# Optimization experiments

Measured on AMD Instinct MI355X. Metric: run time of the kernel, lower is better.

## Reference

```python
import jax, jax.numpy as jnp
import numpy as np

B, T, H, QS = 32, 4096, 512, 512

def setup_inputs() -> dict:
    key = jax.random.key(0)
    k1, k2, k3, k4, k5 = jax.random.split(key, 5)
    query = jax.random.normal(k1, (B, 1, QS), dtype=jnp.float32)
    precomputed_key = jax.random.normal(k2, (B, T, H), dtype=jnp.float32)
    value = jax.random.normal(k3, (B, T, H), dtype=jnp.float32)
    mask = jnp.ones((B, T), dtype=bool)  # unused in original forward
    Wq = jax.random.normal(k4, (H, QS), dtype=jnp.float32) * (1.0 / np.sqrt(QS))
    We = jax.random.normal(k5, (H,), dtype=jnp.float32) * (1.0 / np.sqrt(H))
    return {"query": query, "precomputed_key": precomputed_key, "value": value,
            "mask": mask, "Wq": Wq, "We": We}

def reference(query, precomputed_key, value, mask, Wq, We):
    # query_layer: Linear(query_size -> hidden, no bias): x @ Wq.T
    q = jnp.einsum('bqs,hs->bqh', query, Wq)              # [B,1,H]
    # energy: tanh(q + key) then Linear(hidden -> 1, no bias), squeeze
    scores = jnp.einsum('bth,h->bt', jnp.tanh(q + precomputed_key), We)  # [B,T]
    alphas = jax.nn.softmax(scores, axis=1)               # [B,T]
    # bmm(alphas[B,1,T], value[B,T,D]) -> [B,1,D]
    context = jnp.einsum('bt,btd->bd', alphas, value)[:, None, :]
    return context, alphas
```

## Files before the change

### kernel.cpp

```cpp
#include <hip/hip_runtime.h>
#include <math.h>

#define BB 32
#define TT 4096
#define HH 512
#define QQS 512
#define TS 64
#define CH (TT / TS)

__device__ inline float wave_reduce_sum(float v) {
#pragma unroll
    for (int off = 32; off > 0; off >>= 1) v += __shfl_xor(v, off, 64);
    return v;
}

__device__ inline float fast_tanh(float x) {
    x = fminf(fmaxf(x, -15.f), 15.f);
    float e = __expf(-2.f * x);
    return (1.f - e) / (1.f + e);
}

__global__ void qproj_kernel(const float* __restrict__ query,
                             const float* __restrict__ Wq,
                             float* __restrict__ qout) {
    int wid  = (blockIdx.x * blockDim.x + threadIdx.x) >> 6;
    int lane = threadIdx.x & 63;
    int b = wid >> 9;
    int h = wid & (HH - 1);
    const float4* qr = (const float4*)(query + (size_t)b * QQS);
    const float4* wr = (const float4*)(Wq + (size_t)h * QQS);
    float4 a0 = qr[lane],      w0 = wr[lane];
    float4 a1 = qr[lane + 64], w1 = wr[lane + 64];
    float acc = a0.x * w0.x + a0.y * w0.y + a0.z * w0.z + a0.w * w0.w
              + a1.x * w1.x + a1.y * w1.y + a1.z * w1.z + a1.w * w1.w;
    acc = wave_reduce_sum(acc);
    if (lane == 0) qout[wid] = acc;
}

__global__ void scores_kernel(const float* __restrict__ key,
                              const float* __restrict__ qb,
                              const float* __restrict__ We,
                              float* __restrict__ scores) {
    __shared__ float q_l[HH];
    __shared__ float w_l[HH];
    int row0 = blockIdx.x * 4;
    int b = row0 >> 12;
    q_l[threadIdx.x]       = qb[(size_t)b * HH + threadIdx.x];
    q_l[threadIdx.x + 256] = qb[(size_t)b * HH + threadIdx.x + 256];
    w_l[threadIdx.x]       = We[threadIdx.x];
    w_l[threadIdx.x + 256] = We[threadIdx.x + 256];
    __syncthreads();

    int w = threadIdx.x >> 6, lane = threadIdx.x & 63;
    int row = row0 + w;
    const float4* kr = (const float4*)(key + (size_t)row * HH);
    float4 k0 = kr[lane];
    float4 k1 = kr[lane + 64];
    int h0 = lane * 4, h1 = 256 + lane * 4;
    float p = 0.f;
    p += fast_tanh(q_l[h0 + 0] + k0.x) * w_l[h0 + 0];
    p += fast_tanh(q_l[h0 + 1] + k0.y) * w_l[h0 + 1];
    p += fast_tanh(q_l[h0 + 2] + k0.z) * w_l[h0 + 2];
    p += fast_tanh(q_l[h0 + 3] + k0.w) * w_l[h0 + 3];
    p += fast_tanh(q_l[h1 + 0] + k1.x) * w_l[h1 + 0];
    p += fast_tanh(q_l[h1 + 1] + k1.y) * w_l[h1 + 1];
    p += fast_tanh(q_l[h1 + 2] + k1.z) * w_l[h1 + 2];
    p += fast_tanh(q_l[h1 + 3] + k1.w) * w_l[h1 + 3];
    p = wave_reduce_sum(p);
    if (lane == 0) scores[row] = p;
}

__global__ void softmax_kernel(float* __restrict__ sc) {
    __shared__ float red_max[16];
    __shared__ float red_sum[16];
    float* row = sc + (size_t)blockIdx.x * TT;
    float4 v = ((float4*)row)[threadIdx.x];
    int wv = threadIdx.x >> 6, lane = threadIdx.x & 63;

    float m = fmaxf(fmaxf(v.x, v.y), fmaxf(v.z, v.w));
#pragma unroll
    for (int off = 32; off > 0; off >>= 1) m = fmaxf(m, __shfl_xor(m, off, 64));
    if (lane == 0) red_max[wv] = m;
    __syncthreads();
    m = red_max[0];
#pragma unroll
    for (int i = 1; i < 16; ++i) m = fmaxf(m, red_max[i]);

    float e0 = __expf(v.x - m), e1 = __expf(v.y - m);
    float e2 = __expf(v.z - m), e3 = __expf(v.w - m);
    float s = e0 + e1 + e2 + e3;
    s = wave_reduce_sum(s);
    if (lane == 0) red_sum[wv] = s;
    __syncthreads();
    s = 0.f;
#pragma unroll
    for (int i = 0; i < 16; ++i) s += red_sum[i];
    float inv = 1.f / s;
    ((float4*)row)[threadIdx.x] = make_float4(e0 * inv, e1 * inv, e2 * inv, e3 * inv);
}

__global__ void ctx_partial_kernel(const float* __restrict__ value,
                                   const float* __restrict__ alphas,
                                   float* __restrict__ part) {
    int b = blockIdx.x / TS, ts = blockIdx.x % TS;
    int tid = threadIdx.x;
    const float4* vp = (const float4*)(value + ((size_t)b * TT + (size_t)ts * CH) * HH);
    const float*  ap = alphas + (size_t)b * TT + (size_t)ts * CH;
    float4 acc = make_float4(0.f, 0.f, 0.f, 0.f);
#pragma unroll 4
    for (int r = 0; r < CH; ++r) {
        float a = ap[r];
        float4 v = vp[(size_t)r * (HH / 4) + tid];
        acc.x += a * v.x; acc.y += a * v.y; acc.z += a * v.z; acc.w += a * v.w;
    }
    ((float4*)(part + ((size_t)(ts * BB + b)) * HH))[tid] = acc;
}

__global__ void ctx_reduce_kernel(const float* __restrict__ part,
                                  float* __restrict__ ctx) {
    int i = blockIdx.x * blockDim.x + threadIdx.x;
    float s = 0.f;
#pragma unroll
    for (int ts = 0; ts < TS; ++ts) s += part[(size_t)ts * BB * HH + i];
    ctx[i] = s;
}

extern "C" void kernel_launch(void* const* d_in, const int* in_sizes, int n_in,
                              void* d_out, int out_size, void* d_ws, size_t ws_size,
                              hipStream_t stream) {
    const float* query = (const float*)d_in[0];
    const float* key   = (const float*)d_in[1];
    const float* value = (const float*)d_in[2];
    const float* Wq    = (const float*)d_in[4];
    const float* We    = (const float*)d_in[5];

    float* ctx    = (float*)d_out;
    float* alphas = (float*)d_out + BB * HH;

    float* qbuf = (float*)d_ws;
    float* part = qbuf + BB * HH;

    qproj_kernel<<<(BB * HH) / 4, 256, 0, stream>>>(query, Wq, qbuf);
    scores_kernel<<<(BB * TT) / 4, 256, 0, stream>>>(key, qbuf, We, alphas);
    softmax_kernel<<<BB, 1024, 0, stream>>>(alphas);
    ctx_partial_kernel<<<BB * TS, 128, 0, stream>>>(value, alphas, part);
    ctx_reduce_kernel<<<(BB * HH) / 256, 256, 0, stream>>>(part, ctx);
}
```

Baseline: 126.9 us.

## Fuse scores, chunked online softmax, and context accumulation into one kernel

Replaces the separate scores, softmax, context-partial and reduce kernels with one fused kernel. Each block computes scores for a 64-row chunk, forms a local max and exp-sum, and accumulates unnormalized exp-weighted value partials. A finalize kernel then rescales the partials with the global max and sum and writes the normalized alphas. This removes two launches and the round trips of alphas through global memory between stages, at the cost of fewer blocks (2048 of 256 threads) carrying serial work for both the key and value streams.

```diff
diff --git a/kernel.cpp b/kernel.cpp
--- a/kernel.cpp
+++ b/kernel.cpp
@@ -6,11 +6,17 @@
 #define HH 512
 #define QQS 512
 #define TS 64
-#define CH (TT / TS)
+#define CH 64
 
 __device__ inline float wave_reduce_sum(float v) {
 #pragma unroll
     for (int off = 32; off > 0; off >>= 1) v += __shfl_xor(v, off, 64);
+    return v;
+}
+
+__device__ inline float wave_reduce_max(float v) {
+#pragma unroll
+    for (int off = 32; off > 0; off >>= 1) v = fmaxf(v, __shfl_xor(v, off, 64));
     return v;
 }
 
@@ -37,92 +43,126 @@
     if (lane == 0) qout[wid] = acc;
 }
 
-__global__ void scores_kernel(const float* __restrict__ key,
-                              const float* __restrict__ qb,
-                              const float* __restrict__ We,
-                              float* __restrict__ scores) {
+__global__ __launch_bounds__(256) void fused_kernel(
+        const float* __restrict__ key, const float* __restrict__ value,
+        const float* __restrict__ qb,  const float* __restrict__ We,
+        float* __restrict__ scores, float* __restrict__ mbuf,
+        float* __restrict__ zbuf,   float* __restrict__ part) {
     __shared__ float q_l[HH];
     __shared__ float w_l[HH];
-    int row0 = blockIdx.x * 4;
-    int b = row0 >> 12;
-    q_l[threadIdx.x]       = qb[(size_t)b * HH + threadIdx.x];
-    q_l[threadIdx.x + 256] = qb[(size_t)b * HH + threadIdx.x + 256];
-    w_l[threadIdx.x]       = We[threadIdx.x];
-    w_l[threadIdx.x + 256] = We[threadIdx.x + 256];
+    __shared__ float s_lds[CH];
+    __shared__ float e_lds[CH];
+    __shared__ float ctx_lds[HH];
+
+    int b = blockIdx.x / TS, c = blockIdx.x % TS;
+    int tid = threadIdx.x;
+    q_l[tid]       = qb[(size_t)b * HH + tid];
+    q_l[tid + 256] = qb[(size_t)b * HH + tid + 256];
+    w_l[tid]       = We[tid];
+    w_l[tid + 256] = We[tid + 256];
     __syncthreads();
 
-    int w = threadIdx.x >> 6, lane = threadIdx.x & 63;
-    int row = row0 + w;
-    const float4* kr = (const float4*)(key + (size_t)row * HH);
-    float4 k0 = kr[lane];
-    float4 k1 = kr[lane + 64];
-    int h0 = lane * 4, h1 = 256 + lane * 4;
-    float p = 0.f;
-    p += fast_tanh(q_l[h0 + 0] + k0.x) * w_l[h0 + 0];
-    p += fast_tanh(q_l[h0 + 1] + k0.y) * w_l[h0 + 1];
-    p += fast_tanh(q_l[h0 + 2] + k0.z) * w_l[h0 + 2];
-    p += fast_tanh(q_l[h0 + 3] + k0.w) * w_l[h0 + 3];
-    p += fast_tanh(q_l[h1 + 0] + k1.x) * w_l[h1 + 0];
-    p += fast_tanh(q_l[h1 + 1] + k1.y) * w_l[h1 + 1];
-    p += fast_tanh(q_l[h1 + 2] + k1.z) * w_l[h1 + 2];
-    p += fast_tanh(q_l[h1 + 3] + k1.w) * w_l[h1 + 3];
-    p = wave_reduce_sum(p);
-    if (lane == 0) scores[row] = p;
+    int w = tid >> 6, lane = tid & 63;
+    size_t row0 = (size_t)b * TT + (size_t)c * CH;
+
+    for (int rr = 0; rr < CH / 4; ++rr) {
+        int r = rr * 4 + w;
+        const float4* kr = (const float4*)(key + (row0 + r) * HH);
+        float4 k0 = kr[lane];
+        float4 k1 = kr[lane + 64];
+        int h0 = lane * 4, h1 = 256 + lane * 4;
+        float p = 0.f;
+        p += fast_tanh(q_l[h0 + 0] + k0.x) * w_l[h0 + 0];
+        p += fast_tanh(q_l[h0 + 1] + k0.y) * w_l[h0 + 1];
+        p += fast_tanh(q_l[h0 + 2] + k0.z) * w_l[h0 + 2];
+        p += fast_tanh(q_l[h0 + 3] + k0.w) * w_l[h0 + 3];
+        p += fast_tanh(q_l[h1 + 0] + k1.x) * w_l[h1 + 0];
+        p += fast_tanh(q_l[h1 + 1] + k1.y) * w_l[h1 + 1];
+        p += fast_tanh(q_l[h1 + 2] + k1.z) * w_l[h1 + 2];
+        p += fast_tanh(q_l[h1 + 3] + k1.w) * w_l[h1 + 3];
+        p = wave_reduce_sum(p);
+        if (lane == 0) s_lds[r] = p;
+    }
+    __syncthreads();
+
+    if (w == 0) {
+        float s = s_lds[lane];
+        float m = wave_reduce_max(s);
+        float e = __expf(s - m);
+        e_lds[lane] = e;
+        float z = wave_reduce_sum(e);
+        if (lane == 0) {
+            mbuf[b * TS + c] = m;
+            zbuf[b * TS + c] = z;
+        }
+    } else if (w == 1 && lane < CH / 4) {
+        ((float4*)(scores + row0))[lane] = ((float4*)s_lds)[lane];
+    }
+    __syncthreads();
+
+    int d4 = tid & 127, rg = tid >> 7;
+    const float4* vp = (const float4*)(value + row0 * HH);
+    float4 acc = make_float4(0.f, 0.f, 0.f, 0.f);
+#pragma unroll 4
+    for (int r = rg; r < CH; r += 2) {
+        float a = e_lds[r];
+        float4 v = vp[(size_t)r * (HH / 4) + d4];
+        acc.x += a * v.x; acc.y += a * v.y; acc.z += a * v.z; acc.w += a * v.w;
+    }
+    if (rg == 0) ((float4*)ctx_lds)[d4] = acc;
+    __syncthreads();
+    if (rg == 1) {
+        float4 t = ((float4*)ctx_lds)[d4];
+        t.x += acc.x; t.y += acc.y; t.z += acc.z; t.w += acc.w;
+        ((float4*)(part + ((size_t)c * BB + b) * HH))[d4] = t;
+    }
 }
 
-__global__ void softmax_kernel(float* __restrict__ sc) {
-    __shared__ float red_max[16];
-    __shared__ float red_sum[16];
-    float* row = sc + (size_t)blockIdx.x * TT;
-    float4 v = ((float4*)row)[threadIdx.x];
-    int wv = threadIdx.x >> 6, lane = threadIdx.x & 63;
-
-    float m = fmaxf(fmaxf(v.x, v.y), fmaxf(v.z, v.w));
+__global__ void finalize_kernel(const float* __restrict__ scores,
+                                const float* __restrict__ mbuf,
+                                const float* __restrict__ zbuf,
+                                const float* __restrict__ part,
+                                float* __restrict__ alphas,
+                                float* __restrict__ ctx) {
+    int tid = threadIdx.x, lane = tid & 63;
+    if (blockIdx.x < BB) {
+        int b = blockIdx.x;
+        float m_l = mbuf[b * TS + lane];
+        float z_l = zbuf[b * TS + lane];
+        float M = wave_reduce_max(m_l);
+        float Z = wave_reduce_sum(__expf(m_l - M) * z_l);
+        float invZ = 1.f / Z;
+        const float4* sp = (const float4*)(scores + (size_t)b * TT);
+        float4* ap = (float4*)(alphas + (size_t)b * TT);
 #pragma unroll
-    for (int off = 32; off > 0; off >>= 1) m = fmaxf(m, __shfl_xor(m, off, 64));
-    if (lane == 0) red_max[wv] = m;
-    __syncthreads();
-    m = red_max[0];
+        for (int i = 0; i < 4; ++i) {
+            float4 s = sp[tid + i * 256];
+            float4 a;
+            a.x = __expf(s.x - M) * invZ;
+            a.y = __expf(s.y - M) * invZ;
+            a.z = __expf(s.z - M) * invZ;
+            a.w = __expf(s.w - M) * invZ;
+            ap[tid + i * 256] = a;
+        }
+    } else {
+        int i = blockIdx.x - BB;
+        int b = i >> 1;
+        int d = (i & 1) * 256 + tid;
+        __shared__ float scale[TS];
+        if (tid < TS) {
+            float m_l = mbuf[b * TS + lane];
+            float z_l = zbuf[b * TS + lane];
+            float M = wave_reduce_max(m_l);
+            float Z = wave_reduce_sum(__expf(m_l - M) * z_l);
+            scale[lane] = __expf(m_l - M) / Z;
+        }
+        __syncthreads();
+        float s = 0.f;
 #pragma unroll
-    for (int i = 1; i < 16; ++i) m = fmaxf(m, red_max[i]);
-
-    float e0 = __expf(v.x - m), e1 = __expf(v.y - m);
-    float e2 = __expf(v.z - m), e3 = __expf(v.w - m);
-    float s = e0 + e1 + e2 + e3;
-    s = wave_reduce_sum(s);
-    if (lane == 0) red_sum[wv] = s;
-    __syncthreads();
-    s = 0.f;
-#pragma unroll
-    for (int i = 0; i < 16; ++i) s += red_sum[i];
-    float inv = 1.f / s;
-    ((float4*)row)[threadIdx.x] = make_float4(e0 * inv, e1 * inv, e2 * inv, e3 * inv);
-}
-
-__global__ void ctx_partial_kernel(const float* __restrict__ value,
-                                   const float* __restrict__ alphas,
-                                   float* __restrict__ part) {
-    int b = blockIdx.x / TS, ts = blockIdx.x % TS;
-    int tid = threadIdx.x;
-    const float4* vp = (const float4*)(value + ((size_t)b * TT + (size_t)ts * CH) * HH);
-    const float*  ap = alphas + (size_t)b * TT + (size_t)ts * CH;
-    float4 acc = make_float4(0.f, 0.f, 0.f, 0.f);
-#pragma unroll 4
-    for (int r = 0; r < CH; ++r) {
-        float a = ap[r];
-        float4 v = vp[(size_t)r * (HH / 4) + tid];
-        acc.x += a * v.x; acc.y += a * v.y; acc.z += a * v.z; acc.w += a * v.w;
+        for (int c2 = 0; c2 < TS; ++c2)
+            s += scale[c2] * part[((size_t)c2 * BB + b) * HH + d];
+        ctx[(size_t)b * HH + d] = s;
     }
-    ((float4*)(part + ((size_t)(ts * BB + b)) * HH))[tid] = acc;
-}
-
-__global__ void ctx_reduce_kernel(const float* __restrict__ part,
-                                  float* __restrict__ ctx) {
-    int i = blockIdx.x * blockDim.x + threadIdx.x;
-    float s = 0.f;
-#pragma unroll
-    for (int ts = 0; ts < TS; ++ts) s += part[(size_t)ts * BB * HH + i];
-    ctx[i] = s;
 }
 
 extern "C" void kernel_launch(void* const* d_in, const int* in_sizes, int n_in,
@@ -137,12 +177,13 @@
     float* ctx    = (float*)d_out;
     float* alphas = (float*)d_out + BB * HH;
 
-    float* qbuf = (float*)d_ws;
-    float* part = qbuf + BB * HH;
+    float* qbuf   = (float*)d_ws;
+    float* sc     = qbuf + BB * HH;
+    float* mbuf   = sc + BB * TT;
+    float* zbuf   = mbuf + BB * TS;
+    float* part   = zbuf + BB * TS;
 
     qproj_kernel<<<(BB * HH) / 4, 256, 0, stream>>>(query, Wq, qbuf);
-    scores_kernel<<<(BB * TT) / 4, 256, 0, stream>>>(key, qbuf, We, alphas);
-    softmax_kernel<<<BB, 1024, 0, stream>>>(alphas);
-    ctx_partial_kernel<<<BB * TS, 128, 0, stream>>>(value, alphas, part);
-    ctx_reduce_kernel<<<(BB * HH) / 256, 256, 0, stream>>>(part, ctx);
+    fused_kernel<<<BB * TS, 256, 0, stream>>>(key, value, qbuf, We, sc, mbuf, zbuf, part);
+    finalize_kernel<<<BB + 2 * BB, 256, 0, stream>>>(sc, mbuf, zbuf, part, alphas, ctx);
 }
```

New measurement: 109.0 us. 1.16x faster.
